# Optimization experiments

Hardware: AMD Instinct MI355X
Metric: run time of the kernel (lower is better)

Reference implementation:

```python
import jax, jax.numpy as jnp
import numpy as np


def setup_inputs() -> dict:
    key = jax.random.key(0)
    ks = jax.random.split(key, 14)
    n, c, m, s = 32, 256, 32, 64
    rn = lambda k, shape, sc=1.0: jax.random.normal(k, shape, dtype=jnp.float32) * sc
    return {
        "seg_ori": rn(ks[0], (n, c, m, m)),
        "edge_ori": rn(ks[1], (n, c, m, m)),
        "W_s1": rn(ks[2], (s, c), 0.05), "b_s1": rn(ks[3], (s,), 0.05),
        "W_s11": rn(ks[4], (s, c), 0.05), "b_s11": rn(ks[5], (s,), 0.05),
        "W_mlp": rn(ks[6], (s, c), 0.05), "b_mlp": rn(ks[7], (s,), 0.05),
        "w_s2": rn(ks[8], ()), "b_s2": rn(ks[9], ()),
        "w_s3": rn(ks[10], ()), "b_s3": rn(ks[11], ()),
        "W_g": rn(ks[12], (c, c), 0.02), "b_g": rn(ks[13], (c,), 0.02),
    }


def reference(seg_ori, edge_ori, W_s1, b_s1, W_s11, b_s11, W_mlp, b_mlp,
              w_s2, b_s2, w_s3, b_s3, W_g, b_g):
    n, c, m, _ = seg_ori.shape
    hw = m * m                      # num_n = mids^2
    s = W_s1.shape[0]               # num_s = plane_mid
    seg = seg_ori

    # ---- channel affinity branch ----
    seg_s = jnp.einsum('nchw,sc->nshw', seg, W_s1) + b_s1[None, :, None, None]
    theta_T = seg_s.reshape(n, s, hw)        # view(n, num_s, -1)
    theta = seg_s.reshape(n, hw, s)          # view(n, -1, num_s): reshape, NOT transpose
    ch_att = jax.nn.relu(jnp.mean(seg, axis=(2, 3)) @ W_mlp.T + b_mlp)   # (n, s)
    diag_c = ch_att[:, :, None] * ch_att[:, None, :]                     # (n, s, s) outer
    sim_c = jnp.einsum('nps,nst->npt', theta, diag_c)                    # (n, hw, s)
    sim_c = jax.nn.softmax(jnp.einsum('npt,ntq->npq', sim_c, theta_T), axis=1)  # (n, hw, hw)

    # ---- spatial affinity branch ----
    seg_c = jnp.einsum('nchw,sc->nshw', seg, W_s11) + b_s11[None, :, None, None]
    sigma = seg_c.reshape(n, s, hw)
    sigma_T = seg_c.reshape(n, hw, s)
    sigma_out = jnp.einsum('nps,nsq->npq', sigma_T, sigma)               # (n, hw, hw)
    edge_m = seg * edge_ori
    maxpool_s = jnp.max(seg, axis=1)                                     # (n, m, m)
    edge_m_pool = jnp.max(edge_m, axis=1)                                # (n, m, m)
    seg_ss = (maxpool_s * w_s2 + b_s2).reshape(n, 1, hw)                 # 1x1 conv, 1 channel
    edge_mm = (edge_m_pool * w_s3 + b_s3).reshape(n, hw, 1)
    sim_s = jax.nn.softmax(edge_mm * seg_ss * sigma_out, axis=1)         # (n, hw, hw)

    similarity = sim_c + sim_s

    # ---- GCN: bmm + conv1d(k=1) + relu + residual ----
    seg2 = seg.reshape(n, c, hw)
    seg_sim = jnp.einsum('ncp,npq->ncq', seg2, similarity)               # (n, c, hw)
    out = jax.nn.relu(jnp.einsum('ncl,oc->nol', seg_sim, W_g) + b_g[None, :, None])
    gcn_out = (out + seg2).reshape(n, c, m, m)
    return gcn_out + seg_ori
```

## Files before the change

kernel.cpp:

```cpp
#include <hip/hip_runtime.h>

#define N 32
#define C 256
#define HW 1024
#define S 64
#define LOG2E 1.4426950408889634f

typedef _Float16 f16;
typedef _Float16 f16x4 __attribute__((ext_vector_type(4)));
typedef _Float16 f16x8 __attribute__((ext_vector_type(8)));
typedef float f32x4 __attribute__((ext_vector_type(4)));

#define MFMA(a, b, c) __builtin_amdgcn_mfma_f32_16x16x32_f16(a, b, c, 0, 0, 0)
#define EXP2(x) __builtin_amdgcn_exp2f(x)

__device__ inline f16x8 lds_ld8(const f16* p) {
    return *(const f16x8*)p;
}

__global__ void __launch_bounds__(256) k_pool1(const float* seg, const float* edge,
        f16* segf, float* pms, float* pme, float* mean,
        const float* Ws1, const float* Ws11, const float* Wg, f16* Wf, f16* Wgf) {
    int n = blockIdx.x, cg = blockIdx.y;
    int t = threadIdx.x, w = t >> 6, lane = t & 63;
    int flat = n * 32 + cg;
    if (flat < 256) {
        int i = flat * 256 + t;
        if (i < S * C) { Wf[i] = (f16)Ws1[i]; Wf[S * C + i] = (f16)Ws11[i]; }
        Wgf[i] = (f16)Wg[i];
    }
    int p4 = (lane << 2) + (w << 8);
    size_t base = (size_t)n * C * HW;
    float4 ms = make_float4(-3e38f, -3e38f, -3e38f, -3e38f);
    float4 me = ms;
    __shared__ float psum[4][8];
    for (int ci = 0; ci < 8; ci++) {
        int c = cg * 8 + ci;
        size_t off = base + (size_t)c * HW + p4;
        float4 s = *(const float4*)(seg + off);
        float4 e = *(const float4*)(edge + off);
        union { f16 h[4]; unsigned long long u; } pk;
        pk.h[0] = (f16)s.x; pk.h[1] = (f16)s.y; pk.h[2] = (f16)s.z; pk.h[3] = (f16)s.w;
        *(unsigned long long*)(segf + off) = pk.u;
        ms.x = fmaxf(ms.x, s.x); ms.y = fmaxf(ms.y, s.y);
        ms.z = fmaxf(ms.z, s.z); ms.w = fmaxf(ms.w, s.w);
        me.x = fmaxf(me.x, s.x * e.x); me.y = fmaxf(me.y, s.y * e.y);
        me.z = fmaxf(me.z, s.z * e.z); me.w = fmaxf(me.w, s.w * e.w);
        float sm = s.x + s.y + s.z + s.w;
        for (int o = 32; o; o >>= 1) sm += __shfl_down(sm, o);
        if (lane == 0) psum[w][ci] = sm;
    }
    __syncthreads();
    if (t < 8)
        mean[n * C + cg * 8 + t] =
            (psum[0][t] + psum[1][t] + psum[2][t] + psum[3][t]) * (1.0f / HW);
    size_t pb = ((size_t)n * 32 + cg) * HW + p4;
    *(float4*)(pms + pb) = ms;
    *(float4*)(pme + pb) = me;
}

__global__ void __launch_bounds__(512) k_proj(const f16* segf, const f16* Wf,
        const float* bs1, const float* bs11, const float* mean,
        const float* Wmlp, const float* bmlp,
        const float* pms, const float* pme,
        const float* ws2, const float* bs2, const float* ws3, const float* bs3,
        f16* segc, float* dp2, float* e_, float* dpmm2, float* a2, float* bq) {
    int n = blockIdx.x, qt = blockIdx.y;
    int q0 = qt * 64;
    __shared__ f16 sT[64][264];
    __shared__ f16 pT[64][72];
    __shared__ float cA[S];
    __shared__ float cpart[S][4];
    __shared__ float aP[64][4], bP[64][4];
    const f16* sb = segf + (size_t)n * C * HW + q0;
    int tid = threadIdx.x;
    for (int idx = tid; idx < 2048; idx += 512) {
        int c = idx >> 3, q8 = (idx & 7) << 3;
        f16x8 v = *(const f16x8*)(sb + (size_t)c * HW + q8);
        int cs = c ^ ((idx & 7) << 3);
        for (int j = 0; j < 8; j++) sT[q8 + j][cs] = v[j];
    }
    if (tid < 256) {
        int s = tid >> 2, qp = tid & 3;
        const float* wr = Wmlp + (size_t)s * C + qp * 64;
        const float* mr = mean + (size_t)n * C + qp * 64;
        float acc = 0.f;
        for (int i = 0; i < 64; i++) acc += mr[i] * wr[i];
        cpart[s][qp] = acc;
    } else {
        int idx = tid - 256;
        int ql = idx & 63, g4 = idx >> 6;
        float M = -3e38f, E = -3e38f;
        for (int i = 0; i < 8; i++) {
            int cg = g4 * 8 + i;
            size_t pb = ((size_t)n * 32 + cg) * HW + q0 + ql;
            M = fmaxf(M, pms[pb]);
            E = fmaxf(E, pme[pb]);
        }
        aP[ql][g4] = E; bP[ql][g4] = M;
    }
    __syncthreads();
    if (tid < S) {
        cA[tid] = fmaxf(cpart[tid][0] + cpart[tid][1] + cpart[tid][2]
                        + cpart[tid][3] + bmlp[tid], 0.f);
    } else if (tid >= 448) {
        int ql = tid - 448;
        float E = fmaxf(fmaxf(aP[ql][0], aP[ql][1]), fmaxf(aP[ql][2], aP[ql][3]));
        float M = fmaxf(fmaxf(bP[ql][0], bP[ql][1]), fmaxf(bP[ql][2], bP[ql][3]));
        a2[(size_t)n * HW + q0 + ql] = (E * ws3[0] + bs3[0]) * LOG2E;
        bq[(size_t)n * HW + q0 + ql] = M * ws2[0] + bs2[0];
    }
    int lane = tid & 63, wv = tid >> 6;
    int lm = lane & 15, lg = lane >> 4;
    f32x4 acc[4] = {};
    for (int ck = 0; ck < 8; ck++) {
        int c0 = ck * 32;
        f16x8 a0 = *(const f16x8*)(Wf + (size_t)(wv * 16 + lm) * C + c0 + lg * 8);
        for (int j = 0; j < 4; j++) {
            int row = j * 16 + lm;
            int col = (c0 + lg * 8) ^ ((((row >> 3)) & 7) << 3);
            f16x8 b = lds_ld8(&sT[row][col]);
            acc[j] = MFMA(a0, b, acc[j]);
        }
    }
    for (int rr = 0; rr < 4; rr++) {
        int row = wv * 16 + lg * 4 + rr;
        float bias = (row < S) ? bs1[row] : bs11[row - S];
        for (int j = 0; j < 4; j++) {
            int q = q0 + j * 16 + lm;
            float v = acc[j][rr] + bias;
            if (row < S) pT[row][j * 16 + lm] = (f16)v;
            else         segc[((size_t)n * S + (row - S)) * HW + q] = (f16)v;
        }
    }
    __syncthreads();
    if (tid < 64) {
        float a2c = 0.f;
        for (int t = 0; t < S; t += 8) {
            f16x8 v = lds_ld8(&pT[tid][t]);
            for (int j = 0; j < 8; j++) a2c += (float)v[j] * cA[t + j];
        }
        float d2 = a2c * LOG2E;
        dp2[(size_t)n * HW + 16 * tid + qt] = d2;
        float mx = d2, mn = d2;
        for (int o = 32; o; o >>= 1) {
            mx = fmaxf(mx, __shfl_down(mx, o));
            mn = fminf(mn, __shfl_down(mn, o));
        }
        if (tid == 0) {
            dpmm2[(n * 16 + qt) * 2]     = mx;
            dpmm2[(n * 16 + qt) * 2 + 1] = mn;
        }
    } else if (tid < 128) {
        int ql = tid - 64;
        float a2c = 0.f;
        for (int t = 0; t < S; t++) a2c += cA[t] * (float)pT[t][ql];
        e_[(size_t)n * HW + q0 + ql] = a2c;
    }
}

__global__ void __launch_bounds__(512, 4) k_fused(const f16* segf, const f16* segc,
        const float* dp2, const float* e_, const float* a2, const float* bq,
        const float* dpmm2, const f16* Wgf, const float* bg, float* out) {
    int n = blockIdx.x, q0 = blockIdx.y * 64;
    __shared__ f16 bT[64][72];
    __shared__ f16 wT[2][64][136];
    __shared__ float2 da[HW];
    __shared__ float mred[64][9], lred[64][9];
    __shared__ float msL[64], izsL[64], mcL[64], izcL[64];
    const f16* cb = segc + (size_t)n * S * HW;
    const f16* sb = segf + (size_t)n * C * HW;
    int tid = threadIdx.x;
    for (int idx = tid; idx < 64 * 32; idx += 512) {
        int q = idx & 63, th = (idx >> 6) << 1;
        union { f16 h[2]; unsigned u; } pk;
        pk.h[0] = cb[(size_t)th * HW + q0 + q];
        pk.h[1] = cb[(size_t)(th + 1) * HW + q0 + q];
        *(unsigned*)&bT[q][th] = pk.u;
    }
    for (int i = tid; i < HW; i += 512)
        da[i] = make_float2(dp2[(size_t)n * HW + i], a2[(size_t)n * HW + i]);
    __syncthreads();
    int w = tid >> 6, lane = tid & 63, lm = lane & 15, lg = lane >> 4;
    float ev[4], bqv[4];
    for (int j = 0; j < 4; j++) {
        size_t gq = (size_t)n * HW + q0 + j * 16 + lm;
        ev[j] = e_[gq];  bqv[j] = bq[gq];
    }
    float sm[4], sl[4];
    #pragma unroll
    for (int j = 0; j < 4; j++) { sm[j] = -3e38f; sl[j] = 0.f; }
    for (int chk = 0; chk < 8; chk++) {
        int p0 = chk * 128;
        const f16* sp = cb + (size_t)(p0 + w * 16 + lm) * S;
        f16x8 sa0 = *(const f16x8*)(sp + lg * 8);
        f16x8 sa1 = *(const f16x8*)(sp + 32 + lg * 8);
        float avr[4];
        #pragma unroll
        for (int rr = 0; rr < 4; rr++) avr[rr] = da[p0 + w * 16 + lg * 4 + rr].y;
        #pragma unroll
        for (int j = 0; j < 4; j++) {
            f16x8 bb0 = lds_ld8(&bT[j * 16 + lm][lg * 8]);
            f16x8 bb1 = lds_ld8(&bT[j * 16 + lm][32 + lg * 8]);
            f32x4 sg = {};
            sg = MFMA(sa0, bb0, sg);
            sg = MFMA(sa1, bb1, sg);
            float sc[4], fm = -3e38f;
            #pragma unroll
            for (int rr = 0; rr < 4; rr++) {
                sc[rr] = avr[rr] * bqv[j] * sg[rr];
                fm = fmaxf(fm, sc[rr]);
            }
            float nm = fmaxf(sm[j], fm);
            float fl = 0.f;
            #pragma unroll
            for (int rr = 0; rr < 4; rr++) fl += EXP2(sc[rr] - nm);
            sl[j] = sl[j] * EXP2(sm[j] - nm) + fl;
            sm[j] = nm;
        }
    }
    #pragma unroll
    for (int j = 0; j < 4; j++) {
        #pragma unroll
        for (int o = 16; o <= 32; o <<= 1) {
            float om = __shfl_xor(sm[j], o);
            float ol = __shfl_xor(sl[j], o);
            float nm = fmaxf(sm[j], om);
            sl[j] = sl[j] * EXP2(sm[j] - nm) + ol * EXP2(om - nm);
            sm[j] = nm;
        }
    }
    if (lg == 0)
        #pragma unroll
        for (int j = 0; j < 4; j++) {
            mred[j * 16 + lm][w] = sm[j];
            lred[j * 16 + lm][w] = sl[j];
        }
    {
        float mx = -3e38f, mn = 3e38f;
        for (int j2 = 0; j2 < 16; j2++) {
            mx = fmaxf(mx, dpmm2[(n * 16 + j2) * 2]);
            mn = fminf(mn, dpmm2[(n * 16 + j2) * 2 + 1]);
        }
        int qz = tid >> 3, pi = tid & 7;
        float eqz = e_[(size_t)n * HW + q0 + qz];
        float mzv = (eqz > 0.f) ? eqz * mx : eqz * mn;
        float z0 = 0.f, z1 = 0.f, z2 = 0.f, z3 = 0.f;
        for (int j2 = 0; j2 < 128; j2 += 4) {
            z0 += EXP2(da[pi + 8 * j2].x * eqz - mzv);
            z1 += EXP2(da[pi + 8 * (j2 + 1)].x * eqz - mzv);
            z2 += EXP2(da[pi + 8 * (j2 + 2)].x * eqz - mzv);
            z3 += EXP2(da[pi + 8 * (j2 + 3)].x * eqz - mzv);
        }
        float z = (z0 + z1) + (z2 + z3);
        z += __shfl_xor(z, 1);
        z += __shfl_xor(z, 2);
        z += __shfl_xor(z, 4);
        if (pi == 0) { mcL[qz] = mzv; izcL[qz] = 1.f / z; }
    }
    __syncthreads();
    if (tid < 64) {
        float M = mred[tid][0];
        for (int ww = 1; ww < 8; ww++) M = fmaxf(M, mred[tid][ww]);
        float L = 0.f;
        for (int ww = 0; ww < 8; ww++) L += lred[tid][ww] * EXP2(mred[tid][ww] - M);
        msL[tid] = M; izsL[tid] = 1.f / L;
    }
    __syncthreads();
    float mcv[4], izcv[4], msv[4], izsv[4];
    #pragma unroll
    for (int j = 0; j < 4; j++) {
        int q = j * 16 + lm;
        mcv[j] = mcL[q]; izcv[j] = izcL[q];
        msv[j] = msL[q]; izsv[j] = izsL[q];
    }
    f32x4 acc[2][4] = {};
    for (int chk = 0; chk <= 8; chk++) {
        if (chk > 0) {
            int p0 = (chk - 1) * 128;
            int cur = (chk - 1) & 1;
            #pragma unroll
            for (int ks = 0; ks < 4; ks++) {
                f16x8 a2f[2];
                #pragma unroll
                for (int cf = 0; cf < 2; cf++) {
                    int crow = w * 32 + cf * 16 + lm;
                    a2f[cf] = *(const f16x8*)(sb + (size_t)crow * HW + p0 + ks * 32 + lg * 8);
                }
                #pragma unroll
                for (int qf = 0; qf < 4; qf++) {
                    f16x8 bb = lds_ld8(&wT[cur][qf * 16 + lm][ks * 32 + lg * 8]);
                    acc[0][qf] = MFMA(a2f[0], bb, acc[0][qf]);
                    acc[1][qf] = MFMA(a2f[1], bb, acc[1][qf]);
                }
            }
        }
        if (chk < 8) {
            int p0 = chk * 128;
            const f16* sp = cb + (size_t)(p0 + w * 16 + lm) * S;
            f16x8 sa0 = *(const f16x8*)(sp + lg * 8);
            f16x8 sa1 = *(const f16x8*)(sp + 32 + lg * 8);
            float d2r[4], avr[4];
            #pragma unroll
            for (int rr = 0; rr < 4; rr++) {
                float2 dv = da[p0 + w * 16 + lg * 4 + rr];
                d2r[rr] = dv.x; avr[rr] = dv.y;
            }
            #pragma unroll
            for (int j = 0; j < 4; j++) {
                f16x8 bb0 = lds_ld8(&bT[j * 16 + lm][lg * 8]);
                f16x8 bb1 = lds_ld8(&bT[j * 16 + lm][32 + lg * 8]);
                f32x4 sg = {};
                sg = MFMA(sa0, bb0, sg);
                sg = MFMA(sa1, bb1, sg);
                float wgt[4];
                #pragma unroll
                for (int rr = 0; rr < 4; rr++) {
                    float wc  = EXP2(d2r[rr] * ev[j] - mcv[j]) * izcv[j];
                    float wsv = EXP2(avr[rr] * bqv[j] * sg[rr] - msv[j]) * izsv[j];
                    wgt[rr] = wc + wsv;
                }
                int ql = j * 16 + lm;
                int pp = w * 16 + lg * 4;
                union { f16 h[2]; unsigned u; } c0u, c1u;
                c0u.h[0] = (f16)wgt[0]; c0u.h[1] = (f16)wgt[1];
                c1u.h[0] = (f16)wgt[2]; c1u.h[1] = (f16)wgt[3];
                *(unsigned*)&wT[chk & 1][ql][pp]     = c0u.u;
                *(unsigned*)&wT[chk & 1][ql][pp + 2] = c1u.u;
            }
        }
        __syncthreads();
    }
    f16 (*sT2)[264] = (f16(*)[264])&wT[0][0][0];
    for (int cf = 0; cf < 2; cf++)
        for (int qf = 0; qf < 4; qf++) {
            int crow = w * 32 + cf * 16 + lg * 4;
            int ql = qf * 16 + lm;
            f16x4 pk;
            pk[0] = (f16)acc[cf][qf][0]; pk[1] = (f16)acc[cf][qf][1];
            pk[2] = (f16)acc[cf][qf][2]; pk[3] = (f16)acc[cf][qf][3];
            *(f16x4*)&sT2[ql][crow] = pk;
        }
    __syncthreads();
    int ow = w * 32;
    f32x4 acc2[2][4] = {};
    for (int ck = 0; ck < 8; ck++) {
        int c0 = ck * 32;
        f16x8 af0 = *(const f16x8*)(Wgf + (size_t)(ow + lm) * C + c0 + lg * 8);
        f16x8 af1 = *(const f16x8*)(Wgf + (size_t)(ow + 16 + lm) * C + c0 + lg * 8);
        for (int qf = 0; qf < 4; qf++) {
            f16x8 bf = lds_ld8(&sT2[qf * 16 + lm][c0 + lg * 8]);
            acc2[0][qf] = MFMA(af0, bf, acc2[0][qf]);
            acc2[1][qf] = MFMA(af1, bf, acc2[1][qf]);
        }
    }
    for (int of = 0; of < 2; of++)
        for (int rr = 0; rr < 4; rr++) {
            int o = ow + of * 16 + lg * 4 + rr;
            float bgv = bg[o];
            for (int qf = 0; qf < 4; qf++) {
                int q = q0 + qf * 16 + lm;
                size_t ix = ((size_t)n * C + o) * HW + q;
                out[ix] = fmaxf(acc2[of][qf][rr] + bgv, 0.f) + 2.f * (float)sb[((size_t)o * HW) + q];
            }
        }
}

extern "C" void kernel_launch(void* const* d_in, const int* in_sizes, int n_in,
                              void* d_out, int out_size, void* d_ws, size_t ws_size,
                              hipStream_t stream) {
    const float* seg  = (const float*)d_in[0];
    const float* edge = (const float*)d_in[1];
    const float* Ws1  = (const float*)d_in[2];
    const float* bs1  = (const float*)d_in[3];
    const float* Ws11 = (const float*)d_in[4];
    const float* bs11 = (const float*)d_in[5];
    const float* Wmlp = (const float*)d_in[6];
    const float* bmlp = (const float*)d_in[7];
    const float* ws2  = (const float*)d_in[8];
    const float* bs2  = (const float*)d_in[9];
    const float* ws3  = (const float*)d_in[10];
    const float* bs3  = (const float*)d_in[11];
    const float* Wg   = (const float*)d_in[12];
    const float* bg   = (const float*)d_in[13];
    float* out = (float*)d_out;
    char* wsb = (char*)d_ws;

    f16*   segf   = (f16*)(wsb);
    f16*   segc   = (f16*)(wsb + 16777216);
    float* dpmm2  = (float*)(wsb + 20971520);
    float* pms    = (float*)(wsb + 25165824);
    float* pme    = (float*)(wsb + 29360128);
    f16*   Wf     = (f16*)(wsb + 41943040);
    f16*   Wgf    = (f16*)(wsb + 42008576);
    float* mean   = (float*)(wsb + 42139648);
    float* dp2    = (float*)(wsb + 42180608);
    float* e_     = (float*)(wsb + 42311680);
    float* a2     = (float*)(wsb + 42442752);
    float* bq     = (float*)(wsb + 42573824);

    k_pool1<<<dim3(32, 32), 256, 0, stream>>>(seg, edge, segf, pms, pme, mean,
                                              Ws1, Ws11, Wg, Wf, Wgf);
    k_proj<<<dim3(32, 16), 512, 0, stream>>>(segf, Wf, bs1, bs11, mean,
                                             Wmlp, bmlp, pms, pme,
                                             ws2, bs2, ws3, bs3,
                                             segc, dp2, e_, dpmm2, a2, bq);
    k_fused<<<dim3(32, 16), 512, 0, stream>>>(segf, segc, dp2, e_, a2, bq,
                                              dpmm2, Wgf, bg, out);
}
```

Before: 214.8 us.

## Fuse fp16 conversion and channel max-pooling into projection kernel

Moves the fp16 conversion of seg, the channel max of seg and the channel max of seg*edge out of the first pooling kernel and into the projection kernel. The projection kernel now reads fp32 seg/edge directly, writes segf and fills its LDS tile in the same pass, and reduces the maxima with shuffles and shared memory. This drops the pms/pme intermediate buffers and the separate reread of segf. The first kernel still reads seg for the mean, so seg is read twice. The projection kernel now does more global loading before its MFMA work.

```diff
diff --git a/kernel.cpp b/kernel.cpp
--- a/kernel.cpp
+++ b/kernel.cpp
@@ -18,8 +18,7 @@
     return *(const f16x8*)p;
 }
 
-__global__ void __launch_bounds__(256) k_pool1(const float* seg, const float* edge,
-        f16* segf, float* pms, float* pme, float* mean,
+__global__ void __launch_bounds__(256) k_pool1(const float* seg, float* mean,
         const float* Ws1, const float* Ws11, const float* Wg, f16* Wf, f16* Wgf) {
     int n = blockIdx.x, cg = blockIdx.y;
     int t = threadIdx.x, w = t >> 6, lane = t & 63;
@@ -31,21 +30,10 @@
     }
     int p4 = (lane << 2) + (w << 8);
     size_t base = (size_t)n * C * HW;
-    float4 ms = make_float4(-3e38f, -3e38f, -3e38f, -3e38f);
-    float4 me = ms;
     __shared__ float psum[4][8];
     for (int ci = 0; ci < 8; ci++) {
         int c = cg * 8 + ci;
-        size_t off = base + (size_t)c * HW + p4;
-        float4 s = *(const float4*)(seg + off);
-        float4 e = *(const float4*)(edge + off);
-        union { f16 h[4]; unsigned long long u; } pk;
-        pk.h[0] = (f16)s.x; pk.h[1] = (f16)s.y; pk.h[2] = (f16)s.z; pk.h[3] = (f16)s.w;
-        *(unsigned long long*)(segf + off) = pk.u;
-        ms.x = fmaxf(ms.x, s.x); ms.y = fmaxf(ms.y, s.y);
-        ms.z = fmaxf(ms.z, s.z); ms.w = fmaxf(ms.w, s.w);
-        me.x = fmaxf(me.x, s.x * e.x); me.y = fmaxf(me.y, s.y * e.y);
-        me.z = fmaxf(me.z, s.z * e.z); me.w = fmaxf(me.w, s.w * e.w);
+        float4 s = *(const float4*)(seg + base + (size_t)c * HW + p4);
         float sm = s.x + s.y + s.z + s.w;
         for (int o = 32; o; o >>= 1) sm += __shfl_down(sm, o);
         if (lane == 0) psum[w][ci] = sm;
@@ -54,15 +42,12 @@
     if (t < 8)
         mean[n * C + cg * 8 + t] =
             (psum[0][t] + psum[1][t] + psum[2][t] + psum[3][t]) * (1.0f / HW);
-    size_t pb = ((size_t)n * 32 + cg) * HW + p4;
-    *(float4*)(pms + pb) = ms;
-    *(float4*)(pme + pb) = me;
 }
 
-__global__ void __launch_bounds__(512) k_proj(const f16* segf, const f16* Wf,
+__global__ void __launch_bounds__(512) k_proj(const float* seg, const float* edge,
+        f16* segf, const f16* Wf,
         const float* bs1, const float* bs11, const float* mean,
         const float* Wmlp, const float* bmlp,
-        const float* pms, const float* pme,
         const float* ws2, const float* bs2, const float* ws3, const float* bs3,
         f16* segc, float* dp2, float* e_, float* dpmm2, float* a2, float* bq) {
     int n = blockIdx.x, qt = blockIdx.y;
@@ -71,14 +56,53 @@
     __shared__ f16 pT[64][72];
     __shared__ float cA[S];
     __shared__ float cpart[S][4];
-    __shared__ float aP[64][4], bP[64][4];
-    const f16* sb = segf + (size_t)n * C * HW + q0;
+    __shared__ float psS[8][64], psE[8][64];
+    const float* sgp = seg  + (size_t)n * C * HW + q0;
+    const float* egp = edge + (size_t)n * C * HW + q0;
+    f16*         sfp = segf + (size_t)n * C * HW + q0;
     int tid = threadIdx.x;
-    for (int idx = tid; idx < 2048; idx += 512) {
-        int c = idx >> 3, q8 = (idx & 7) << 3;
-        f16x8 v = *(const f16x8*)(sb + (size_t)c * HW + q8);
-        int cs = c ^ ((idx & 7) << 3);
-        for (int j = 0; j < 8; j++) sT[q8 + j][cs] = v[j];
+    int f4 = tid & 15;
+    {
+        float4 ms = make_float4(-3e38f, -3e38f, -3e38f, -3e38f);
+        float4 me = ms;
+        #pragma unroll
+        for (int k = 0; k < 8; k++) {
+            int c = (tid >> 4) + 32 * k;
+            size_t off = (size_t)c * HW + (f4 << 2);
+            float4 s = *(const float4*)(sgp + off);
+            float4 e = *(const float4*)(egp + off);
+            union { f16 h[4]; unsigned long long u; } pk;
+            pk.h[0] = (f16)s.x; pk.h[1] = (f16)s.y;
+            pk.h[2] = (f16)s.z; pk.h[3] = (f16)s.w;
+            *(unsigned long long*)(sfp + off) = pk.u;
+            int cs = c ^ (((f4 >> 1) & 7) << 3);
+            sT[f4 * 4 + 0][cs] = pk.h[0];
+            sT[f4 * 4 + 1][cs] = pk.h[1];
+            sT[f4 * 4 + 2][cs] = pk.h[2];
+            sT[f4 * 4 + 3][cs] = pk.h[3];
+            ms.x = fmaxf(ms.x, s.x); ms.y = fmaxf(ms.y, s.y);
+            ms.z = fmaxf(ms.z, s.z); ms.w = fmaxf(ms.w, s.w);
+            me.x = fmaxf(me.x, s.x * e.x); me.y = fmaxf(me.y, s.y * e.y);
+            me.z = fmaxf(me.z, s.z * e.z); me.w = fmaxf(me.w, s.w * e.w);
+        }
+        #pragma unroll
+        for (int o = 16; o <= 32; o <<= 1) {
+            ms.x = fmaxf(ms.x, __shfl_xor(ms.x, o));
+            ms.y = fmaxf(ms.y, __shfl_xor(ms.y, o));
+            ms.z = fmaxf(ms.z, __shfl_xor(ms.z, o));
+            ms.w = fmaxf(ms.w, __shfl_xor(ms.w, o));
+            me.x = fmaxf(me.x, __shfl_xor(me.x, o));
+            me.y = fmaxf(me.y, __shfl_xor(me.y, o));
+            me.z = fmaxf(me.z, __shfl_xor(me.z, o));
+            me.w = fmaxf(me.w, __shfl_xor(me.w, o));
+        }
+        int wv0 = tid >> 6, lane0 = tid & 63;
+        if (lane0 < 16) {
+            psS[wv0][f4 * 4 + 0] = ms.x; psS[wv0][f4 * 4 + 1] = ms.y;
+            psS[wv0][f4 * 4 + 2] = ms.z; psS[wv0][f4 * 4 + 3] = ms.w;
+            psE[wv0][f4 * 4 + 0] = me.x; psE[wv0][f4 * 4 + 1] = me.y;
+            psE[wv0][f4 * 4 + 2] = me.z; psE[wv0][f4 * 4 + 3] = me.w;
+        }
     }
     if (tid < 256) {
         int s = tid >> 2, qp = tid & 3;
@@ -87,28 +111,20 @@
         float acc = 0.f;
         for (int i = 0; i < 64; i++) acc += mr[i] * wr[i];
         cpart[s][qp] = acc;
-    } else {
-        int idx = tid - 256;
-        int ql = idx & 63, g4 = idx >> 6;
-        float M = -3e38f, E = -3e38f;
-        for (int i = 0; i < 8; i++) {
-            int cg = g4 * 8 + i;
-            size_t pb = ((size_t)n * 32 + cg) * HW + q0 + ql;
-            M = fmaxf(M, pms[pb]);
-            E = fmaxf(E, pme[pb]);
-        }
-        aP[ql][g4] = E; bP[ql][g4] = M;
     }
     __syncthreads();
     if (tid < S) {
         cA[tid] = fmaxf(cpart[tid][0] + cpart[tid][1] + cpart[tid][2]
                         + cpart[tid][3] + bmlp[tid], 0.f);
     } else if (tid >= 448) {
-        int ql = tid - 448;
-        float E = fmaxf(fmaxf(aP[ql][0], aP[ql][1]), fmaxf(aP[ql][2], aP[ql][3]));
-        float M = fmaxf(fmaxf(bP[ql][0], bP[ql][1]), fmaxf(bP[ql][2], bP[ql][3]));
-        a2[(size_t)n * HW + q0 + ql] = (E * ws3[0] + bs3[0]) * LOG2E;
-        bq[(size_t)n * HW + q0 + ql] = M * ws2[0] + bs2[0];
+        int q = tid - 448;
+        float M = -3e38f, E = -3e38f;
+        for (int ww = 0; ww < 8; ww++) {
+            M = fmaxf(M, psS[ww][q]);
+            E = fmaxf(E, psE[ww][q]);
+        }
+        a2[(size_t)n * HW + q0 + q] = (E * ws3[0] + bs3[0]) * LOG2E;
+        bq[(size_t)n * HW + q0 + q] = M * ws2[0] + bs2[0];
     }
     int lane = tid & 63, wv = tid >> 6;
     int lm = lane & 15, lg = lane >> 4;
@@ -389,8 +405,6 @@
     f16*   segf   = (f16*)(wsb);
     f16*   segc   = (f16*)(wsb + 16777216);
     float* dpmm2  = (float*)(wsb + 20971520);
-    float* pms    = (float*)(wsb + 25165824);
-    float* pme    = (float*)(wsb + 29360128);
     f16*   Wf     = (f16*)(wsb + 41943040);
     f16*   Wgf    = (f16*)(wsb + 42008576);
     float* mean   = (float*)(wsb + 42139648);
@@ -399,10 +413,9 @@
     float* a2     = (float*)(wsb + 42442752);
     float* bq     = (float*)(wsb + 42573824);
 
-    k_pool1<<<dim3(32, 32), 256, 0, stream>>>(seg, edge, segf, pms, pme, mean,
-                                              Ws1, Ws11, Wg, Wf, Wgf);
-    k_proj<<<dim3(32, 16), 512, 0, stream>>>(segf, Wf, bs1, bs11, mean,
-                                             Wmlp, bmlp, pms, pme,
+    k_pool1<<<dim3(32, 32), 256, 0, stream>>>(seg, mean, Ws1, Ws11, Wg, Wf, Wgf);
+    k_proj<<<dim3(32, 16), 512, 0, stream>>>(seg, edge, segf, Wf, bs1, bs11,
+                                             mean, Wmlp, bmlp,
                                              ws2, bs2, ws3, bs3,
                                              segc, dp2, e_, dpmm2, a2, bq);
     k_fused<<<dim3(32, 16), 512, 0, stream>>>(segf, segc, dp2, e_, a2, bq,
```

Result: no change. 213.0 us (-0.8%).
